# Kernel optimization log

Measured on AMD Instinct MI355X. Metric: run time of the kernel, lower is better.

Reference implementation:

```python
import jax, jax.numpy as jnp
import numpy as np

N_NODES = 50000
N_EDGES = 800000
IN_DIM = 64
HEADS = 8
DHEAD = 8
CLAMP = 5.0


def _xavier(key, shape, fan_in, fan_out):
    std = jnp.sqrt(2.0 / (fan_in + fan_out))
    return std * jax.random.normal(key, shape, dtype=jnp.float32)


def setup_inputs() -> dict:
    key = jax.random.key(0)
    ks = jax.random.split(key, 12)
    HD = HEADS * DHEAD
    x = jax.random.normal(ks[0], (N_NODES, IN_DIM), dtype=jnp.float32)
    edge_attr = jax.random.normal(ks[1], (N_EDGES, IN_DIM), dtype=jnp.float32)
    edge_index = jax.random.randint(ks[2], (2, N_EDGES), 0, N_NODES, dtype=jnp.int32)
    # Linear weights stored as [in, out] so y = x @ W + b
    WQ = _xavier(ks[3], (IN_DIM, HD), IN_DIM, HD)
    bQ = jnp.zeros((HD,), jnp.float32)
    WK = _xavier(ks[4], (IN_DIM, HD), IN_DIM, HD)
    bK = jnp.zeros((HD,), jnp.float32)
    WE = _xavier(ks[5], (IN_DIM, 2 * HD), IN_DIM, 2 * HD)
    bE = jnp.zeros((2 * HD,), jnp.float32)
    WV = _xavier(ks[6], (IN_DIM, HD), IN_DIM, HD)
    bV = jnp.zeros((HD,), jnp.float32)
    Aw = _xavier(ks[7], (DHEAD, HEADS, 1), DHEAD * HEADS, 1)
    VeRow = _xavier(ks[8], (DHEAD, HEADS, DHEAD), DHEAD * HEADS, DHEAD)
    return {"x": x, "edge_attr": edge_attr, "edge_index": edge_index,
            "WQ": WQ, "bQ": bQ, "WK": WK, "bK": bK, "WE": WE, "bE": bE,
            "WV": WV, "bV": bV, "Aw": Aw, "VeRow": VeRow}


def _forward(x, edge_attr, edge_index, WQ, bQ, WK, bK, WE, bE, WV, bV, Aw, VeRow):
    N = x.shape[0]
    src_idx = edge_index[0]
    dst_idx = edge_index[1]
    Q_h = (x @ WQ + bQ).reshape(N, HEADS, DHEAD)
    K_h = (x @ WK + bK).reshape(N, HEADS, DHEAD)
    V_h = (x @ WV + bV).reshape(N, HEADS, DHEAD)
    E = (edge_attr @ WE + bE).reshape(-1, HEADS, 2 * DHEAD)  # [E,H,2D]
    E_w, E_b = E[:, :, :DHEAD], E[:, :, DHEAD:]
    # per-edge score: gather + signed-sqrt transform
    score = K_h[src_idx] + Q_h[dst_idx]              # [E,H,D]
    score = score * E_w
    score = jnp.sqrt(jax.nn.relu(score)) - jnp.sqrt(jax.nn.relu(-score))
    score = score + E_b                               # act = Identity
    e_t = score
    wE = score.reshape(score.shape[0], HEADS * DHEAD)
    # attention logits: contract over head dim with Aw -> [E,H,1]
    logit = jnp.einsum('ehd,dhc->ehc', score, Aw)
    logit = jnp.clip(logit, -CLAMP, CLAMP)
    # segment softmax over destination nodes (pyg_softmax)
    smax = jax.ops.segment_max(logit, dst_idx, num_segments=N)
    ex = jnp.exp(logit - smax[dst_idx])
    denom = jax.ops.segment_sum(ex, dst_idx, num_segments=N)[dst_idx] + 1e-16
    attn = ex / denom                                 # [E,H,1], dropout p=0
    # message passing: scatter-add weighted values
    msg = V_h[src_idx] * attn                         # [E,H,D]
    wV = jax.ops.segment_sum(msg, dst_idx, num_segments=N)
    # edge enhancement
    rowV = jax.ops.segment_sum(e_t * attn, dst_idx, num_segments=N)  # [N,H,D]
    wV = wV + jnp.einsum('nhd,dhc->nhc', rowV, VeRow)
    return wV, wE


def reference(x, edge_attr, edge_index, WQ, bQ, WK, bK, WE, bE, WV, bV, Aw, VeRow):
    return _forward(x, edge_attr, edge_index, WQ, bQ, WK, bK, WE, bE, WV, bV, Aw, VeRow)
```

## Files before the change

kernel.cpp:

```cpp
#include <hip/hip_runtime.h>
#include <hip/hip_bf16.h>
#include <math.h>

#define N_NODES 50000
#define N_EDGES 800000
#define CLAMP_V 5.0f

typedef short short8 __attribute__((ext_vector_type(8)));
typedef short short4v __attribute__((ext_vector_type(4)));
typedef float f32x4  __attribute__((ext_vector_type(4)));

static __device__ inline short f2bf(float x) {
    __hip_bfloat16 h = __float2bfloat16(x);
    return __builtin_bit_cast(short, h);
}
static __device__ inline float bf2f(short s) {
    unsigned u = ((unsigned)(unsigned short)s) << 16;
    return __builtin_bit_cast(float, u);
}

__global__ __launch_bounds__(256) void qkv_kernel(
    const float* __restrict__ x,
    const float* __restrict__ WQ, const float* __restrict__ bQ,
    const float* __restrict__ WK, const float* __restrict__ bK,
    const float* __restrict__ WV, const float* __restrict__ bV,
    float* __restrict__ Q, float* __restrict__ K, float* __restrict__ V)
{
    const int t = threadIdx.x;
    const int c = t & 63;
    const int nl = t >> 6;
    const int base = blockIdx.x * 16;

    float accQ[4], accK[4], accV[4];
    int nodes[4];
#pragma unroll
    for (int j = 0; j < 4; ++j) {
        nodes[j] = base + j * 4 + nl;
        accQ[j] = bQ[c]; accK[j] = bK[c]; accV[j] = bV[c];
    }
    for (int k = 0; k < 64; ++k) {
        const float wq = WQ[k * 64 + c];
        const float wk = WK[k * 64 + c];
        const float wv = WV[k * 64 + c];
#pragma unroll
        for (int j = 0; j < 4; ++j) {
            const float xv = x[nodes[j] * 64 + k];
            accQ[j] += xv * wq;
            accK[j] += xv * wk;
            accV[j] += xv * wv;
        }
    }
#pragma unroll
    for (int j = 0; j < 4; ++j) {
        const int n = nodes[j];
        Q[n * 64 + c] = accQ[j];
        K[n * 64 + c] = accK[j];
        V[n * 64 + c] = accV[j];
    }
}

__global__ __launch_bounds__(256, 3) void edge_kernel(
    const float* __restrict__ edge_attr,
    const int* __restrict__ src_idx, const int* __restrict__ dst_idx,
    const float* __restrict__ WE, const float* __restrict__ bE,
    const float* __restrict__ Aw,
    const float* __restrict__ Qn, const float* __restrict__ Kn,
    const float* __restrict__ Vn, const float* __restrict__ VeRow,
    float* __restrict__ wE_out, float* __restrict__ denom,
    float* __restrict__ wV_num)
{
    __shared__ __align__(16) char raw[49408];
    __shared__ float bEs[128];

    short8* Bhi = (short8*)raw;
    short8* Blo = (short8*)(raw + 16384);

    const int t = threadIdx.x;
    const int wave = t >> 6;
    const int lane = t & 63;

    short* BhiE = (short*)raw;
    short* BloE = (short*)(raw + 16384);
    for (int i = t; i < 8192; i += 256) {
        const int j  = i & 7;
        const int ln = (i >> 3) & 63;
        const int kh = (i >> 9) & 1;
        const int ct = i >> 10;
        const int k   = kh * 32 + ((ln >> 4) << 3) + j;
        const int col = (ct << 4) + (ln & 15);
        const float w = WE[k * 128 + col];
        const short hb = f2bf(w);
        BhiE[i] = hb;
        BloE[i] = f2bf(w - bf2f(hb));
    }
    if (t < 128) bEs[t] = bE[t];
    __syncthreads();

    unsigned short* Eb = (unsigned short*)(raw + 32768 + wave * 4160);

    const int h    = lane >> 3;
    const int kk   = lane & 7;
    const int g    = lane >> 4;
    const int c4   = lane & 15;
    const int h16k = (h << 4) + kk;
    const int ewbase = (h16k << 4) + (h << 2);
    const int ebbase = ((h16k + 8) << 4) + (h << 2);

    float veR[8], awR[8];
#pragma unroll
    for (int dd = 0; dd < 8; ++dd) {
        veR[dd] = VeRow[dd * 64 + lane];
        awR[dd] = Aw[dd * 8 + h];
    }

    const int G = (int)gridDim.x;

    float4 arC[4], arN[4];
    int seC[16], deC[16], seN[16], deN[16];

    int it = blockIdx.x;
    {
        const int ebase0 = __builtin_amdgcn_readfirstlane(it * 64 + wave * 16);
#pragma unroll
        for (int p = 0; p < 2; ++p) {
            const float* srcp = edge_attr + (size_t)(ebase0 + c4) * 64 + p * 32 + (g << 3);
            arC[2 * p]     = *(const float4*)srcp;
            arC[2 * p + 1] = *(const float4*)(srcp + 4);
        }
#pragma unroll
        for (int r = 0; r < 16; ++r) {
            seC[r] = src_idx[ebase0 + r];
            deC[r] = dst_idx[ebase0 + r];
        }
    }

    for (; it < 12500; it += G) {
        const int ebaseC = __builtin_amdgcn_readfirstlane(it * 64 + wave * 16);
        const int itN    = it + G;
        const int itNc   = (itN < 12500) ? itN : 0;
        const int ebaseN = __builtin_amdgcn_readfirstlane(itNc * 64 + wave * 16);

        short8 ah[2], al[2];
#pragma unroll
        for (int p = 0; p < 2; ++p) {
            const float xv[8] = {arC[2*p].x, arC[2*p].y, arC[2*p].z, arC[2*p].w,
                                 arC[2*p+1].x, arC[2*p+1].y, arC[2*p+1].z, arC[2*p+1].w};
#pragma unroll
            for (int j = 0; j < 8; ++j) {
                const short hb = f2bf(xv[j]);
                ah[p][j] = hb;
                al[p][j] = f2bf(xv[j] - bf2f(hb));
            }
        }

#pragma unroll
        for (int r = 0; r < 16; ++r) {
            seN[r] = src_idx[ebaseN + r];
            deN[r] = dst_idx[ebaseN + r];
        }

        float vv[16], kv[16], qv[16];
#pragma unroll
        for (int r = 0; r < 16; ++r) vv[r] = Vn[seC[r] * 64 + lane];
#pragma unroll
        for (int r = 0; r < 16; ++r) {
            kv[r] = Kn[seC[r] * 64 + lane];
            qv[r] = Qn[deC[r] * 64 + lane];
        }

#pragma unroll
        for (int p = 0; p < 2; ++p) {
            const float* srcp = edge_attr + (size_t)(ebaseN + c4) * 64 + p * 32 + (g << 3);
            arN[2 * p]     = *(const float4*)srcp;
            arN[2 * p + 1] = *(const float4*)(srcp + 4);
        }

        f32x4 acc[8] = {};
        __builtin_amdgcn_s_setprio(1);
#pragma unroll
        for (int kh = 0; kh < 2; ++kh) {
#pragma unroll
            for (int ct = 0; ct < 8; ++ct) {
                const short8 bh = Bhi[(ct * 2 + kh) * 64 + lane];
                const short8 bl = Blo[(ct * 2 + kh) * 64 + lane];
                acc[ct] = __builtin_amdgcn_mfma_f32_16x16x32_bf16(ah[kh], bh, acc[ct], 0, 0, 0);
                acc[ct] = __builtin_amdgcn_mfma_f32_16x16x32_bf16(al[kh], bh, acc[ct], 0, 0, 0);
                acc[ct] = __builtin_amdgcn_mfma_f32_16x16x32_bf16(ah[kh], bl, acc[ct], 0, 0, 0);
            }
        }
        __builtin_amdgcn_s_setprio(0);

#pragma unroll
        for (int ct = 0; ct < 8; ++ct) {
            const int col = (ct << 4) + c4;
            const float b = bEs[col];
            short4v pk;
#pragma unroll
            for (int rr = 0; rr < 4; ++rr) pk[rr] = f2bf(acc[ct][rr] + b);
            *(short4v*)(Eb + (col << 4) + (ct << 2) + (g << 2)) = pk;
        }
        __asm__ volatile("s_waitcnt lgkmcnt(0)" ::: "memory");
        __builtin_amdgcn_sched_barrier(0);

#pragma unroll
        for (int idx = 0; idx < 16; ++idx) {
            const int e = ebaseC + idx;
            const int d = deC[idx];
            const float kq = kv[idx] + qv[idx];
            const float ew = bf2f((short)Eb[ewbase + idx]);
            const float eb = bf2f((short)Eb[ebbase + idx]);
            float sc = kq * ew;
            sc = copysignf(sqrtf(fabsf(sc)), sc) + eb;
            wE_out[(size_t)e * 64 + lane] = sc;

            float rsum = 0.f, pp = 0.f;
#pragma unroll
            for (int dd = 0; dd < 8; ++dd) {
                const float etd = __shfl(sc, (lane & 56) + dd);
                rsum += etd * veR[dd];
                pp   += etd * awR[dd];
            }
            pp = fminf(fmaxf(pp, -CLAMP_V), CLAMP_V);
            const float ex = __expf(pp);
            if (kk == 0) unsafeAtomicAdd(&denom[d * 8 + h], ex);
            unsafeAtomicAdd(&wV_num[(size_t)d * 64 + lane],
                            ex * (vv[idx] + rsum));
        }
        __builtin_amdgcn_sched_barrier(0);

#pragma unroll
        for (int p = 0; p < 4; ++p) arC[p] = arN[p];
#pragma unroll
        for (int r = 0; r < 16; ++r) { seC[r] = seN[r]; deC[r] = deN[r]; }
    }
}

__global__ __launch_bounds__(256) void finalize_kernel(
    const float* __restrict__ denom, float* __restrict__ wV)
{
    const int i = blockIdx.x * 256 + threadIdx.x;
    const int n = i >> 6;
    const int h = (i >> 3) & 7;
    const float dn = denom[n * 8 + h] + 1e-16f;
    wV[i] = wV[i] / dn;
}

extern "C" void kernel_launch(void* const* d_in, const int* in_sizes, int n_in,
                              void* d_out, int out_size, void* d_ws, size_t ws_size,
                              hipStream_t stream) {
    const float* x         = (const float*)d_in[0];
    const float* edge_attr = (const float*)d_in[1];
    const int*   ei        = (const int*)  d_in[2];
    const float* WQ = (const float*)d_in[3];
    const float* bQ = (const float*)d_in[4];
    const float* WK = (const float*)d_in[5];
    const float* bK = (const float*)d_in[6];
    const float* WE = (const float*)d_in[7];
    const float* bE = (const float*)d_in[8];
    const float* WV = (const float*)d_in[9];
    const float* bV = (const float*)d_in[10];
    const float* Aw = (const float*)d_in[11];
    const float* VeRow = (const float*)d_in[12];

    float* out    = (float*)d_out;
    float* wV_out = out;
    float* wE_out = out + (size_t)N_NODES * 64;

    float* ws    = (float*)d_ws;
    float* Q     = ws;
    float* K     = ws + 3200000;
    float* V     = ws + 6400000;
    float* denom = ws + 9600000;

    const int* src_idx = ei;
    const int* dst_idx = ei + N_EDGES;

    hipMemsetAsync(wV_out, 0, (size_t)N_NODES * 64 * sizeof(float), stream);
    hipMemsetAsync(denom, 0, (size_t)N_NODES * 8 * sizeof(float), stream);

    qkv_kernel<<<3125, 256, 0, stream>>>(x, WQ, bQ, WK, bK, WV, bV, Q, K, V);
    edge_kernel<<<768, 256, 0, stream>>>(edge_attr, src_idx, dst_idx, WE, bE, Aw,
                                         Q, K, V, VeRow, wE_out, denom, wV_out);
    finalize_kernel<<<12500, 256, 0, stream>>>(denom, wV_out);
}
```

Before: 319.1 us.

## Use per-wave atomic work queue for edge chunks and vectorize finalize

Replaces the static grid-stride loop in the edge kernel with a dynamic work queue: each wave atomically grabs 16-edge chunks from a global counter, prefetching the next chunk while processing the current one. This aims to even out load across waves and CUs, at the cost of one global atomic per chunk per wave and an extra memset. The finalize kernel now processes four floats per thread with a reciprocal multiply, using a quarter of the blocks.

```diff
diff --git a/kernel.cpp b/kernel.cpp
--- a/kernel.cpp
+++ b/kernel.cpp
@@ -4,6 +4,7 @@
 
 #define N_NODES 50000
 #define N_EDGES 800000
+#define N_CHUNKS 50000
 #define CLAMP_V 5.0f
 
 typedef short short8 __attribute__((ext_vector_type(8)));
@@ -67,7 +68,7 @@
     const float* __restrict__ Qn, const float* __restrict__ Kn,
     const float* __restrict__ Vn, const float* __restrict__ VeRow,
     float* __restrict__ wE_out, float* __restrict__ denom,
-    float* __restrict__ wV_num)
+    float* __restrict__ wV_num, int* __restrict__ wq_counter)
 {
     __shared__ __align__(16) char raw[49408];
     __shared__ float bEs[128];
@@ -113,14 +114,19 @@
         awR[dd] = Aw[dd * 8 + h];
     }
 
-    const int G = (int)gridDim.x;
+    auto fetch_chunk = [&]() -> int {
+        int v = 0;
+        if (lane == 0) v = atomicAdd(wq_counter, 1);
+        return __builtin_amdgcn_readfirstlane(__shfl(v, 0));
+    };
 
     float4 arC[4], arN[4];
     int seC[16], deC[16], seN[16], deN[16];
 
-    int it = blockIdx.x;
+    int cC = fetch_chunk();
+    if (cC >= N_CHUNKS) return;
     {
-        const int ebase0 = __builtin_amdgcn_readfirstlane(it * 64 + wave * 16);
+        const int ebase0 = cC << 4;
 #pragma unroll
         for (int p = 0; p < 2; ++p) {
             const float* srcp = edge_attr + (size_t)(ebase0 + c4) * 64 + p * 32 + (g << 3);
@@ -134,11 +140,11 @@
         }
     }
 
-    for (; it < 12500; it += G) {
-        const int ebaseC = __builtin_amdgcn_readfirstlane(it * 64 + wave * 16);
-        const int itN    = it + G;
-        const int itNc   = (itN < 12500) ? itN : 0;
-        const int ebaseN = __builtin_amdgcn_readfirstlane(itNc * 64 + wave * 16);
+    while (true) {
+        const int ebaseC = cC << 4;
+        const int cN     = fetch_chunk();
+        const int cNc    = (cN < N_CHUNKS) ? cN : 0;
+        const int ebaseN = cNc << 4;
 
         short8 ah[2], al[2];
 #pragma unroll
@@ -228,6 +234,8 @@
         }
         __builtin_amdgcn_sched_barrier(0);
 
+        if (cN >= N_CHUNKS) break;
+        cC = cN;
 #pragma unroll
         for (int p = 0; p < 4; ++p) arC[p] = arN[p];
 #pragma unroll
@@ -238,11 +246,14 @@
 __global__ __launch_bounds__(256) void finalize_kernel(
     const float* __restrict__ denom, float* __restrict__ wV)
 {
-    const int i = blockIdx.x * 256 + threadIdx.x;
-    const int n = i >> 6;
-    const int h = (i >> 3) & 7;
-    const float dn = denom[n * 8 + h] + 1e-16f;
-    wV[i] = wV[i] / dn;
+    const int i4 = blockIdx.x * 256 + threadIdx.x;
+    const int base = i4 << 2;
+    const int n = base >> 6;
+    const int h = (base >> 3) & 7;
+    const float inv = 1.0f / (denom[n * 8 + h] + 1e-16f);
+    float4 v = *(float4*)(wV + base);
+    v.x *= inv; v.y *= inv; v.z *= inv; v.w *= inv;
+    *(float4*)(wV + base) = v;
 }
 
 extern "C" void kernel_launch(void* const* d_in, const int* in_sizes, int n_in,
@@ -271,15 +282,17 @@
     float* K     = ws + 3200000;
     float* V     = ws + 6400000;
     float* denom = ws + 9600000;
+    int*   wqc   = (int*)(ws + 10000000);
 
     const int* src_idx = ei;
     const int* dst_idx = ei + N_EDGES;
 
     hipMemsetAsync(wV_out, 0, (size_t)N_NODES * 64 * sizeof(float), stream);
     hipMemsetAsync(denom, 0, (size_t)N_NODES * 8 * sizeof(float), stream);
+    hipMemsetAsync(wqc, 0, sizeof(int), stream);
 
     qkv_kernel<<<3125, 256, 0, stream>>>(x, WQ, bQ, WK, bK, WV, bV, Q, K, V);
     edge_kernel<<<768, 256, 0, stream>>>(edge_attr, src_idx, dst_idx, WE, bE, Aw,
-                                         Q, K, V, VeRow, wE_out, denom, wV_out);
-    finalize_kernel<<<12500, 256, 0, stream>>>(denom, wV_out);
-}
+                                         Q, K, V, VeRow, wE_out, denom, wV_out, wqc);
+    finalize_kernel<<<3125, 256, 0, stream>>>(denom, wV_out);
+}
```

Measured after the change: 778.1 us. 2.44x slower.
